# Performance work log

Hardware: AMD Instinct MI355X
Metric: run time of the kernel (lower is better)

## Reference

```python
import jax, jax.numpy as jnp
import numpy as np

B = 4        # number of point clouds (equal-size contiguous batches)
P = 8192     # points per cloud
C_IN = 64
C_OUT = 64
K = 16       # kNN neighbors (includes the point itself, as in PyG knn)
EPS = 1e-5
NEG_SLOPE = 0.2


def setup_inputs() -> dict:
    key = jax.random.key(0)
    k1, k2, k3 = jax.random.split(key, 3)
    x = jax.random.normal(k1, (B * P, C_IN), dtype=jnp.float32)
    batch = jnp.repeat(jnp.arange(B, dtype=jnp.int64), P)  # sorted, equal sizes
    W = jax.random.normal(k2, (2 * C_IN, C_OUT), dtype=jnp.float32) * (1.0 / np.sqrt(2 * C_IN))
    b = jax.random.normal(k3, (C_OUT,), dtype=jnp.float32) * 0.01
    gamma = jnp.ones((C_OUT,), dtype=jnp.float32)
    beta = jnp.zeros((C_OUT,), dtype=jnp.float32)
    return {"x": x, "batch": batch, "W": W, "b": b, "gamma": gamma, "beta": beta}


def _edgeconv(x, W, b, gamma, beta):
    xb = x.reshape(B, P, C_IN)
    # per-cloud pairwise squared distances: [B, P, P]
    sq = jnp.sum(xb * xb, axis=-1)
    d = sq[:, :, None] + sq[:, None, :] - 2.0 * jnp.einsum("bpc,bqc->bpq", xb, xb)
    # k nearest neighbors (smallest distance, self included)
    _, idx = jax.lax.top_k(-d, K)                      # [B, P, K]
    xj = jax.vmap(lambda pts, ind: pts[ind])(xb, idx)  # [B, P, K, C_IN]
    xi = xb[:, :, None, :]
    e = jnp.concatenate([jnp.broadcast_to(xi, xj.shape), xj - xi], axis=-1)  # [B,P,K,2C]
    # edge MLP: Linear -> BatchNorm1d (training-mode batch stats over all edges) -> LeakyReLU
    h = jnp.einsum("bpke,eo->bpko", e, W) + b          # [B, P, K, C_OUT]
    hf = h.reshape(-1, C_OUT)
    mean = jnp.mean(hf, axis=0)
    var = jnp.mean(hf * hf, axis=0) - mean * mean      # biased variance (torch BN)
    hn = (h - mean) * jax.lax.rsqrt(var + EPS) * gamma + beta
    a = jnp.where(hn >= 0, hn, NEG_SLOPE * hn)
    # max aggregation over neighbors
    return jnp.max(a, axis=2).reshape(B * P, C_OUT)


def reference(x, batch, W, b, gamma, beta):
    # `batch` encodes B equal-size contiguous clouds; kNN is computed per cloud.
    return _edgeconv(x, W, b, gamma, beta)
```

## Files before the change

### kernel.cpp

```cpp
#include <hip/hip_runtime.h>
#include <cfloat>

#define BATCH 4
#define P 8192
#define C 64
#define KNN 16
#define NPTS (BATCH * P)
#define NEDGE (NPTS * KNN)
#define EPSV 1e-5f
#define SLOPE 0.2f
#define NQ 2
#define QCOLS (P / NQ)
#define QCAP 8

typedef __attribute__((ext_vector_type(8))) short bf16x8;
typedef __attribute__((ext_vector_type(16))) float f32x16;


__device__ __forceinline__ unsigned short f2bf(float f) {
    unsigned u = __float_as_uint(f);
    u += 0x7FFFu + ((u >> 16) & 1u);
    return (unsigned short)(u >> 16);
}
__device__ __forceinline__ float bf2f(unsigned short s) {
    return __uint_as_float(((unsigned)s) << 16);
}
__device__ __forceinline__ unsigned monof(float f) {
    unsigned u = __float_as_uint(f);
    return u ^ ((unsigned)((int)u >> 31) | 0x80000000u);
}
__device__ __forceinline__ float invmonof(unsigned k) {
    unsigned u = (k & 0x80000000u) ? (k ^ 0x80000000u) : ~k;
    return __uint_as_float(u);
}

__global__ void prep_frag(const float* __restrict__ x, uint4* __restrict__ xfh,
                          uint4* __restrict__ xfm, uint4* __restrict__ xfl,
                          float* __restrict__ sq) {
    __shared__ float part[32][9];
    int tid = threadIdx.x;
    int ptl = tid >> 3, j8 = tid & 7;
    int g = blockIdx.x;
    int p = g * 32 + ptl;
    const float4* xp = (const float4*)(x + (size_t)p * C + j8 * 8);
    float4 a = xp[0], b = xp[1];
    float v[8] = {a.x, a.y, a.z, a.w, b.x, b.y, b.z, b.w};
    unsigned short hs[8], ms[8], ls[8];
    float ssum = 0.f;
#pragma unroll
    for (int e = 0; e < 8; ++e) {
        float xv = v[e];
        ssum = fmaf(xv, xv, ssum);
        unsigned short h = f2bf(xv);
        float r1 = xv - bf2f(h);
        unsigned short m = f2bf(r1);
        float r2 = r1 - bf2f(m);
        unsigned short l = f2bf(r2);
        hs[e] = h; ms[e] = m; ls[e] = l;
    }
    int dst = (g * 4 + (j8 >> 1)) * 64 + ptl + 32 * (j8 & 1);
    uint4 ph, pm, pl;
    ph.x = (unsigned)hs[0] | ((unsigned)hs[1] << 16);
    ph.y = (unsigned)hs[2] | ((unsigned)hs[3] << 16);
    ph.z = (unsigned)hs[4] | ((unsigned)hs[5] << 16);
    ph.w = (unsigned)hs[6] | ((unsigned)hs[7] << 16);
    pm.x = (unsigned)ms[0] | ((unsigned)ms[1] << 16);
    pm.y = (unsigned)ms[2] | ((unsigned)ms[3] << 16);
    pm.z = (unsigned)ms[4] | ((unsigned)ms[5] << 16);
    pm.w = (unsigned)ms[6] | ((unsigned)ms[7] << 16);
    pl.x = (unsigned)ls[0] | ((unsigned)ls[1] << 16);
    pl.y = (unsigned)ls[2] | ((unsigned)ls[3] << 16);
    pl.z = (unsigned)ls[4] | ((unsigned)ls[5] << 16);
    pl.w = (unsigned)ls[6] | ((unsigned)ls[7] << 16);
    xfh[dst] = ph; xfm[dst] = pm; xfl[dst] = pl;
    part[ptl][j8] = ssum;
    __syncthreads();
    if (j8 == 0) {
        float s = 0.f;
#pragma unroll
        for (int k = 0; k < 8; ++k) s += part[ptl][k];
        sq[p] = s;
    }
}

#define SORTED_INS16(MV, IDV)                                                  \
    {                                                                          \
        float _m = (MV); int _id = (IDV);                                      \
        bool c0 = _m < tv[0], c1 = _m < tv[1], c2 = _m < tv[2],                \
             c3 = _m < tv[3], c4 = _m < tv[4], c5 = _m < tv[5],                \
             c6 = _m < tv[6], c7 = _m < tv[7], c8 = _m < tv[8],                \
             c9 = _m < tv[9], c10 = _m < tv[10], c11 = _m < tv[11],            \
             c12 = _m < tv[12], c13 = _m < tv[13], c14 = _m < tv[14],          \
             c15 = _m < tv[15];                                                \
        tv[15] = c15 ? (c14 ? tv[14] : _m) : tv[15];                           \
        ti[15] = c15 ? (c14 ? ti[14] : _id) : ti[15];                          \
        tv[14] = c14 ? (c13 ? tv[13] : _m) : tv[14];                           \
        ti[14] = c14 ? (c13 ? ti[13] : _id) : ti[14];                          \
        tv[13] = c13 ? (c12 ? tv[12] : _m) : tv[13];                           \
        ti[13] = c13 ? (c12 ? ti[12] : _id) : ti[13];                          \
        tv[12] = c12 ? (c11 ? tv[11] : _m) : tv[12];                           \
        ti[12] = c12 ? (c11 ? ti[11] : _id) : ti[12];                          \
        tv[11] = c11 ? (c10 ? tv[10] : _m) : tv[11];                           \
        ti[11] = c11 ? (c10 ? ti[10] : _id) : ti[11];                          \
        tv[10] = c10 ? (c9 ? tv[9] : _m) : tv[10];                             \
        ti[10] = c10 ? (c9 ? ti[9] : _id) : ti[10];                            \
        tv[9] = c9 ? (c8 ? tv[8] : _m) : tv[9];                                \
        ti[9] = c9 ? (c8 ? ti[8] : _id) : ti[9];                               \
        tv[8] = c8 ? (c7 ? tv[7] : _m) : tv[8];                                \
        ti[8] = c8 ? (c7 ? ti[7] : _id) : ti[8];                               \
        tv[7] = c7 ? (c6 ? tv[6] : _m) : tv[7];                                \
        ti[7] = c7 ? (c6 ? ti[6] : _id) : ti[7];                               \
        tv[6] = c6 ? (c5 ? tv[5] : _m) : tv[6];                                \
        ti[6] = c6 ? (c5 ? ti[5] : _id) : ti[6];                               \
        tv[5] = c5 ? (c4 ? tv[4] : _m) : tv[5];                                \
        ti[5] = c5 ? (c4 ? ti[4] : _id) : ti[5];                               \
        tv[4] = c4 ? (c3 ? tv[3] : _m) : tv[4];                                \
        ti[4] = c4 ? (c3 ? ti[3] : _id) : ti[4];                               \
        tv[3] = c3 ? (c2 ? tv[2] : _m) : tv[3];                                \
        ti[3] = c3 ? (c2 ? ti[2] : _id) : ti[3];                               \
        tv[2] = c2 ? (c1 ? tv[1] : _m) : tv[2];                                \
        ti[2] = c2 ? (c1 ? ti[1] : _id) : ti[2];                               \
        tv[1] = c1 ? (c0 ? tv[0] : _m) : tv[1];                                \
        ti[1] = c1 ? (c0 ? ti[0] : _id) : ti[1];                               \
        tv[0] = c0 ? _m : tv[0];                                               \
        ti[0] = c0 ? _id : ti[0];                                              \
    }

#define DRAIN_Q                                                                \
    {                                                                          \
        _Pragma("nounroll")                                                    \
        for (int j = 0; j < QCAP; ++j) {                                       \
            unsigned long long kq = q[j * 256 + tid];                          \
            bool valid = (j < qn);                                             \
            float dv = valid ? __uint_as_float((unsigned)(kq >> 32)) : FLT_MAX;\
            int di = (int)(unsigned)(kq & 0xFFFFFFFFu);                        \
            SORTED_INS16(dv, di)                                               \
        }                                                                      \
        qn = 0;                                                                \
    }

__global__ __launch_bounds__(256, 4) void knn_kernel(const uint4* __restrict__ xfh,
                                                     const uint4* __restrict__ xfm,
                                                     const uint4* __restrict__ xfl,
                                                     const float* __restrict__ sq,
                                                     float* __restrict__ pv,
                                                     int* __restrict__ pi) {
    __shared__ unsigned long long smem[64 * 65];
    unsigned long long* q = smem;
    unsigned long long (*fink)[65] = (unsigned long long (*)[65])smem;

    int tid = threadIdx.x;
    int b = blockIdx.x & 3;
    int t = blockIdx.x >> 2;
    int tile = t & 127;
    int half = t >> 7;
    int bglob = b * P;
    int r0 = tile * 64;
    int w = tid >> 6, lane = tid & 63;
    int wr = w & 1, wc = w >> 1;
    int hi = lane >> 5;
    int rloc = lane & 31;

    int gA = ((bglob + r0) >> 5) + wr;
    bf16x8 Rh[4], Rm[4], Rl[4];
#pragma unroll
    for (int kk = 0; kk < 4; ++kk) {
        Rh[kk] = __builtin_bit_cast(bf16x8, xfh[(gA * 4 + kk) * 64 + lane]);
        Rm[kk] = __builtin_bit_cast(bf16x8, xfm[(gA * 4 + kk) * 64 + lane]);
        Rl[kk] = __builtin_bit_cast(bf16x8, xfl[(gA * 4 + kk) * 64 + lane]);
    }

    float tv[16];
    int   ti[16];
#pragma unroll
    for (int j = 0; j < 16; ++j) { tv[j] = FLT_MAX; ti[j] = 0; }
    int qn = 0;

    int cw0 = half * QCOLS + wc * 2048;

    for (int chunk = 0; chunk < 64; ++chunk) {
        int c0 = cw0 + chunk * 32;
        int gB = (bglob + c0) >> 5;
        const uint4* ch = &xfh[(gB * 4) * 64 + lane];
        const uint4* cm = &xfm[(gB * 4) * 64 + lane];
        const uint4* cl = &xfl[(gB * 4) * 64 + lane];

        f32x16 acc0, acc1;
#pragma unroll
        for (int i = 0; i < 16; ++i) { acc0[i] = 0.f; acc1[i] = 0.f; }
#pragma unroll
        for (int kk = 0; kk < 4; ++kk) {
            bf16x8 Ch = __builtin_bit_cast(bf16x8, ch[kk * 64]);
            bf16x8 Cm = __builtin_bit_cast(bf16x8, cm[kk * 64]);
            bf16x8 Cl = __builtin_bit_cast(bf16x8, cl[kk * 64]);
            acc0 = __builtin_amdgcn_mfma_f32_32x32x16_bf16(Ch, Rh[kk], acc0, 0, 0, 0);
            acc1 = __builtin_amdgcn_mfma_f32_32x32x16_bf16(Ch, Rm[kk], acc1, 0, 0, 0);
            acc0 = __builtin_amdgcn_mfma_f32_32x32x16_bf16(Cm, Rh[kk], acc0, 0, 0, 0);
            acc1 = __builtin_amdgcn_mfma_f32_32x32x16_bf16(Cm, Rm[kk], acc1, 0, 0, 0);
            acc0 = __builtin_amdgcn_mfma_f32_32x32x16_bf16(Ch, Rl[kk], acc0, 0, 0, 0);
            acc1 = __builtin_amdgcn_mfma_f32_32x32x16_bf16(Cl, Rh[kk], acc1, 0, 0, 0);
        }

        int cb = c0 + 4 * hi;
        float4 sqA[4];
#pragma unroll
        for (int g4 = 0; g4 < 4; ++g4)
            sqA[g4] = *(const float4*)(&sq[bglob + cb + g4 * 8]);
        int bgc = bglob + cb;

#pragma unroll
        for (int reg = 0; reg < 16; ++reg) {
            float s = fmaf(-2.f, acc0[reg] + acc1[reg],
                           ((const float*)&sqA[reg >> 2])[reg & 3]);
            if (__any(qn == QCAP)) { DRAIN_Q }
            bool pass = s < tv[15];
            if (pass) {
                int cid = bgc + (reg & 3) + 8 * (reg >> 2);
                unsigned long long kk =
                    ((unsigned long long)__float_as_uint(s) << 32) | (unsigned)cid;
                q[qn * 256 + tid] = kk;
                qn += 1;
            }
        }
    }

    DRAIN_Q

    __syncthreads();

    {
        int rowl = 32 * wr + rloc;
        int li = wc * 2 + hi;
#pragma unroll
        for (int j = 0; j < 16; ++j)
            fink[rowl][li * 16 + j] =
                ((unsigned long long)monof(tv[j]) << 32) | (unsigned)ti[j];
    }
    __syncthreads();
    if (tid < 128) {
        int row = tid & 63, pr = tid >> 6;
        int base = pr * 32;
        unsigned long long tk[16];
#pragma unroll
        for (int j = 0; j < 16; ++j) tk[j] = fink[row][base + j];
        unsigned long long worstk = tk[0];
#pragma unroll
        for (int j = 1; j < 16; ++j) worstk = (tk[j] > worstk) ? tk[j] : worstk;
        for (int e = 0; e < 16; ++e) {
            unsigned long long k = fink[row][base + 16 + e];
            if (k < worstk) {
                unsigned long long mx = tk[0]; int pos = 0;
#pragma unroll
                for (int j = 1; j < 16; ++j) {
                    bool g = tk[j] > mx; mx = g ? tk[j] : mx; pos = g ? j : pos;
                }
#pragma unroll
                for (int j = 0; j < 16; ++j)
                    if (j == pos) tk[j] = k;
                unsigned long long nw = tk[0];
#pragma unroll
                for (int j = 1; j < 16; ++j) nw = (tk[j] > nw) ? tk[j] : nw;
                worstk = nw;
            }
        }
#pragma unroll
        for (int j = 0; j < 16; ++j) fink[row][base + j] = tk[j];
    }
    __syncthreads();
    if (tid < 64) {
        int row = tid;
        unsigned long long tk[16];
#pragma unroll
        for (int j = 0; j < 16; ++j) tk[j] = fink[row][j];
        unsigned long long worstk = tk[0];
#pragma unroll
        for (int j = 1; j < 16; ++j) worstk = (tk[j] > worstk) ? tk[j] : worstk;
        for (int e = 0; e < 16; ++e) {
            unsigned long long k = fink[row][32 + e];
            if (k < worstk) {
                unsigned long long mx = tk[0]; int pos = 0;
#pragma unroll
                for (int j = 1; j < 16; ++j) {
                    bool g = tk[j] > mx; mx = g ? tk[j] : mx; pos = g ? j : pos;
                }
#pragma unroll
                for (int j = 0; j < 16; ++j)
                    if (j == pos) tk[j] = k;
                unsigned long long nw = tk[0];
#pragma unroll
                for (int j = 1; j < 16; ++j) nw = (tk[j] > nw) ? tk[j] : nw;
                worstk = nw;
            }
        }
        size_t o = (((size_t)(bglob + r0 + row)) * NQ + half) * KNN;
#pragma unroll
        for (int j = 0; j < 16; ++j) {
            pv[o + j] = invmonof((unsigned)(tk[j] >> 32));
            pi[o + j] = (int)(unsigned)(tk[j] & 0xFFFFFFFFu);
        }
    }
}

__global__ void merge_kernel(const float* __restrict__ pv, const int* __restrict__ pi,
                             int* __restrict__ idx_out) {
    __shared__ unsigned long long mk[128 * 33];
    int tid = threadIdx.x;
    int lr = tid & 127, q = tid >> 7;
    int row = blockIdx.x * 128 + lr;
    size_t o = ((size_t)row * NQ + q) * KNN;
#pragma unroll
    for (int j = 0; j < 16; ++j) {
        mk[lr * 33 + q * 16 + j] =
            ((unsigned long long)monof(pv[o + j]) << 32) | (unsigned)pi[o + j];
    }
    __syncthreads();
    if (tid < 128) {
        unsigned long long tk[16];
#pragma unroll
        for (int j = 0; j < 16; ++j) tk[j] = mk[tid * 33 + j];
        unsigned long long worstk = tk[0];
#pragma unroll
        for (int j = 1; j < 16; ++j) worstk = (tk[j] > worstk) ? tk[j] : worstk;
        for (int e = 16; e < 32; ++e) {
            unsigned long long k = mk[tid * 33 + e];
            if (k < worstk) {
                unsigned long long mx = tk[0]; int pos = 0;
#pragma unroll
                for (int j = 1; j < 16; ++j) {
                    bool g = tk[j] > mx; mx = g ? tk[j] : mx; pos = g ? j : pos;
                }
#pragma unroll
                for (int j = 0; j < 16; ++j)
                    if (j == pos) tk[j] = k;
                unsigned long long nw = tk[0];
#pragma unroll
                for (int j = 1; j < 16; ++j) nw = (tk[j] > nw) ? tk[j] : nw;
                worstk = nw;
            }
        }
        size_t oo = (size_t)tid * KNN + (size_t)blockIdx.x * 128 * KNN;
#pragma unroll
        for (int j = 0; j < 16; ++j)
            idx_out[oo + j] = (int)(unsigned)(tk[j] & 0xFFFFFFFFu);
    }
}

__global__ void prep_UV(const float* __restrict__ x, const float* __restrict__ W,
                        float* __restrict__ U, float* __restrict__ V) {
    __shared__ float Ws[128][64];
    __shared__ float xs[4][64];
    int tid = threadIdx.x;
    for (int i = tid; i < 128 * 64; i += 256) ((float*)Ws)[i] = W[i];
    int p0 = blockIdx.x * 4;
    int r = tid >> 6, c = tid & 63;
    xs[r][c] = x[(size_t)(p0 + r) * C + c];
    __syncthreads();
    float u = 0.f, v = 0.f;
#pragma unroll
    for (int k = 0; k < 64; ++k) {
        float xv = xs[r][k];
        float w1 = Ws[k][c];
        float w2 = Ws[64 + k][c];
        u = fmaf(xv, w1 - w2, u);
        v = fmaf(xv, w2, v);
    }
    size_t o = (size_t)(p0 + r) * C + c;
    U[o] = u;
    V[o] = v;
}

__global__ void stats_kernel(const float* __restrict__ U, const float* __restrict__ V,
                             const float* __restrict__ bias, const int* __restrict__ idx,
                             float* __restrict__ stats) {
    int tid = threadIdx.x;
    int c = tid & 63, kk = tid >> 6;
    int p0 = blockIdx.x * 32;
    float bc = bias[c];
    float sum = 0.f, sumsq = 0.f;
    for (int pp = 0; pp < 32; ++pp) {
        int p = p0 + pp;
        float u = U[(size_t)p * C + c] + bc;
#pragma unroll
        for (int k4 = 0; k4 < 4; ++k4) {
            int j = idx[(size_t)p * KNN + kk * 4 + k4];
            float h = u + V[(size_t)j * C + c];
            sum += h;
            sumsq = fmaf(h, h, sumsq);
        }
    }
    __shared__ float red[2][4][64];
    red[0][kk][c] = sum;
    red[1][kk][c] = sumsq;
    __syncthreads();
    if (tid < 64) {
        float s = red[0][0][tid] + red[0][1][tid] + red[0][2][tid] + red[0][3][tid];
        atomicAdd(&stats[tid], s);
    } else if (tid < 128) {
        int cc = tid - 64;
        float s = red[1][0][cc] + red[1][1][cc] + red[1][2][cc] + red[1][3][cc];
        atomicAdd(&stats[64 + cc], s);
    }
}

__global__ void finalize_kernel(const float* __restrict__ stats,
                                const float* __restrict__ gamma,
                                const float* __restrict__ beta,
                                float* __restrict__ sshift) {
    int c = threadIdx.x;
    const float N = (float)NEDGE;
    float mean = stats[c] / N;
    float var = stats[64 + c] / N - mean * mean;
    float s = gamma[c] * rsqrtf(var + EPSV);
    sshift[c] = s;
    sshift[64 + c] = beta[c] - mean * s;
}

__global__ void out_kernel(const float* __restrict__ U, const float* __restrict__ V,
                           const float* __restrict__ bias, const int* __restrict__ idx,
                           const float* __restrict__ sshift, float* __restrict__ out) {
    int tid = threadIdx.x;
    int c = tid & 63, g = tid >> 6;
    int p0 = blockIdx.x * 16;
    float s = sshift[c], t = sshift[64 + c];
    float bc = bias[c];
    for (int pp = g; pp < 16; pp += 4) {
        int p = p0 + pp;
        float mx = -FLT_MAX, mn = FLT_MAX;
#pragma unroll
        for (int k = 0; k < KNN; ++k) {
            int j = idx[(size_t)p * KNN + k];
            float v = V[(size_t)j * C + c];
            mx = fmaxf(mx, v);
            mn = fminf(mn, v);
        }
        float hsel = (s >= 0.f) ? mx : mn;
        float hn = fmaf(s, U[(size_t)p * C + c] + bc + hsel, t);
        out[(size_t)p * C + c] = (hn >= 0.f) ? hn : SLOPE * hn;
    }
}

extern "C" void kernel_launch(void* const* d_in, const int* in_sizes, int n_in,
                              void* d_out, int out_size, void* d_ws, size_t ws_size,
                              hipStream_t stream) {
    const float* x     = (const float*)d_in[0];
    const float* W     = (const float*)d_in[2];
    const float* bias  = (const float*)d_in[3];
    const float* gamma = (const float*)d_in[4];
    const float* beta  = (const float*)d_in[5];
    float* out = (float*)d_out;

    float* wsf    = (float*)d_ws;
    float* U      = wsf;
    float* V      = wsf + 2097152;
    uint4* xfh    = (uint4*)wsf;
    uint4* xfm    = (uint4*)(wsf + 1048576);
    uint4* xfl    = (uint4*)(wsf + 2097152);
    float* sq     = wsf + 4194304;
    float* stats  = wsf + 4227072;
    float* sshift = wsf + 4227200;
    int*   idx    = (int*)(wsf + 4227328);
    float* pv     = wsf + 4751616;
    int*   pi     = (int*)(wsf + 5800192);

    hipLaunchKernelGGL(prep_frag, dim3(NPTS / 32), dim3(256), 0, stream, x, xfh, xfm, xfl, sq);
    hipLaunchKernelGGL(knn_kernel, dim3(BATCH * (P / 64) * NQ), dim3(256), 0, stream,
                       (const uint4*)xfh, (const uint4*)xfm, (const uint4*)xfl, sq, pv, pi);
    hipLaunchKernelGGL(merge_kernel, dim3(NPTS / 128), dim3(256), 0, stream, pv, pi, idx);
    hipLaunchKernelGGL(prep_UV, dim3(NPTS / 4), dim3(256), 0, stream, x, W, U, V);
    hipMemsetAsync(stats, 0, 128 * sizeof(float), stream);
    hipLaunchKernelGGL(stats_kernel, dim3(NPTS / 32), dim3(256), 0, stream, U, V, bias, idx, stats);
    hipLaunchKernelGGL(finalize_kernel, dim3(1), dim3(64), 0, stream, stats, gamma, beta, sshift);
    hipLaunchKernelGGL(out_kernel, dim3(NPTS / 16), dim3(256), 0, stream, U, V, bias, idx, sshift, out);
}
```

Baseline: 509.7 us.

## Compute neighbor max/min during stats pass and fold finalize into output kernel

The stats kernel now also tracks per-channel max and min of the gathered V values over the 16 neighbors and writes the pre-normalization selected value to a buffer. It picks max or min from the sign of gamma, since the rsqrt factor is positive. The output kernel no longer re-gathers V through idx. It becomes an elementwise float4 normalize plus LeakyReLU, and each block recomputes the scale and shift itself, which removes the separate finalize launch. In exchange it writes and reads an extra 8 MB hsel buffer, which reuses the pv workspace region.

```diff
diff --git a/kernel.cpp b/kernel.cpp
--- a/kernel.cpp
+++ b/kernel.cpp
@@ -370,27 +370,35 @@
 }
 
 __global__ void stats_kernel(const float* __restrict__ U, const float* __restrict__ V,
-                             const float* __restrict__ bias, const int* __restrict__ idx,
-                             float* __restrict__ stats) {
-    int tid = threadIdx.x;
-    int c = tid & 63, kk = tid >> 6;
+                             const float* __restrict__ bias,
+                             const float* __restrict__ gamma,
+                             const int* __restrict__ idx,
+                             float* __restrict__ stats, float* __restrict__ hsel) {
+    int tid = threadIdx.x;
+    int c = tid & 63, g = tid >> 6;
     int p0 = blockIdx.x * 32;
     float bc = bias[c];
+    bool gpos = (gamma[c] >= 0.f);
     float sum = 0.f, sumsq = 0.f;
-    for (int pp = 0; pp < 32; ++pp) {
+    for (int pp = g; pp < 32; pp += 4) {
         int p = p0 + pp;
         float u = U[(size_t)p * C + c] + bc;
-#pragma unroll
-        for (int k4 = 0; k4 < 4; ++k4) {
-            int j = idx[(size_t)p * KNN + kk * 4 + k4];
-            float h = u + V[(size_t)j * C + c];
+        float mx = -FLT_MAX, mn = FLT_MAX;
+#pragma unroll
+        for (int k = 0; k < KNN; ++k) {
+            int j = idx[(size_t)p * KNN + k];
+            float v = V[(size_t)j * C + c];
+            float h = u + v;
             sum += h;
             sumsq = fmaf(h, h, sumsq);
-        }
+            mx = fmaxf(mx, v);
+            mn = fminf(mn, v);
+        }
+        hsel[(size_t)p * C + c] = u + (gpos ? mx : mn);
     }
     __shared__ float red[2][4][64];
-    red[0][kk][c] = sum;
-    red[1][kk][c] = sumsq;
+    red[0][g][c] = sum;
+    red[1][g][c] = sumsq;
     __syncthreads();
     if (tid < 64) {
         float s = red[0][0][tid] + red[0][1][tid] + red[0][2][tid] + red[0][3][tid];
@@ -402,40 +410,38 @@
     }
 }
 
-__global__ void finalize_kernel(const float* __restrict__ stats,
-                                const float* __restrict__ gamma,
-                                const float* __restrict__ beta,
-                                float* __restrict__ sshift) {
-    int c = threadIdx.x;
-    const float N = (float)NEDGE;
-    float mean = stats[c] / N;
-    float var = stats[64 + c] / N - mean * mean;
-    float s = gamma[c] * rsqrtf(var + EPSV);
-    sshift[c] = s;
-    sshift[64 + c] = beta[c] - mean * s;
-}
-
-__global__ void out_kernel(const float* __restrict__ U, const float* __restrict__ V,
-                           const float* __restrict__ bias, const int* __restrict__ idx,
-                           const float* __restrict__ sshift, float* __restrict__ out) {
-    int tid = threadIdx.x;
-    int c = tid & 63, g = tid >> 6;
-    int p0 = blockIdx.x * 16;
-    float s = sshift[c], t = sshift[64 + c];
-    float bc = bias[c];
-    for (int pp = g; pp < 16; pp += 4) {
-        int p = p0 + pp;
-        float mx = -FLT_MAX, mn = FLT_MAX;
-#pragma unroll
-        for (int k = 0; k < KNN; ++k) {
-            int j = idx[(size_t)p * KNN + k];
-            float v = V[(size_t)j * C + c];
-            mx = fmaxf(mx, v);
-            mn = fminf(mn, v);
-        }
-        float hsel = (s >= 0.f) ? mx : mn;
-        float hn = fmaf(s, U[(size_t)p * C + c] + bc + hsel, t);
-        out[(size_t)p * C + c] = (hn >= 0.f) ? hn : SLOPE * hn;
+__global__ void out_kernel(const float* __restrict__ hsel,
+                           const float* __restrict__ stats,
+                           const float* __restrict__ gamma,
+                           const float* __restrict__ beta,
+                           float* __restrict__ out) {
+    __shared__ float sS[64], sT[64];
+    int tid = threadIdx.x;
+    if (tid < 64) {
+        const float N = (float)NEDGE;
+        float mean = stats[tid] / N;
+        float var = stats[64 + tid] / N - mean * mean;
+        float s = gamma[tid] * rsqrtf(var + EPSV);
+        sS[tid] = s;
+        sT[tid] = beta[tid] - mean * s;
+    }
+    __syncthreads();
+    int gid = blockIdx.x * 256 + tid;
+#pragma unroll
+    for (int r = 0; r < 2; ++r) {
+        size_t i4 = (size_t)gid + (size_t)r * 262144;
+        size_t i = i4 * 4;
+        int c0 = (int)(i & 63);
+        float4 h4 = *(const float4*)&hsel[i];
+        float4 s4 = *(const float4*)&sS[c0];
+        float4 t4 = *(const float4*)&sT[c0];
+        float4 o4;
+        float hn;
+        hn = fmaf(s4.x, h4.x, t4.x); o4.x = (hn >= 0.f) ? hn : SLOPE * hn;
+        hn = fmaf(s4.y, h4.y, t4.y); o4.y = (hn >= 0.f) ? hn : SLOPE * hn;
+        hn = fmaf(s4.z, h4.z, t4.z); o4.z = (hn >= 0.f) ? hn : SLOPE * hn;
+        hn = fmaf(s4.w, h4.w, t4.w); o4.w = (hn >= 0.f) ? hn : SLOPE * hn;
+        *(float4*)&out[i] = o4;
     }
 }
 
@@ -457,10 +463,10 @@
     uint4* xfl    = (uint4*)(wsf + 2097152);
     float* sq     = wsf + 4194304;
     float* stats  = wsf + 4227072;
-    float* sshift = wsf + 4227200;
     int*   idx    = (int*)(wsf + 4227328);
     float* pv     = wsf + 4751616;
     int*   pi     = (int*)(wsf + 5800192);
+    float* hsel   = wsf + 4751616;
 
     hipLaunchKernelGGL(prep_frag, dim3(NPTS / 32), dim3(256), 0, stream, x, xfh, xfm, xfl, sq);
     hipLaunchKernelGGL(knn_kernel, dim3(BATCH * (P / 64) * NQ), dim3(256), 0, stream,
@@ -468,7 +474,8 @@
     hipLaunchKernelGGL(merge_kernel, dim3(NPTS / 128), dim3(256), 0, stream, pv, pi, idx);
     hipLaunchKernelGGL(prep_UV, dim3(NPTS / 4), dim3(256), 0, stream, x, W, U, V);
     hipMemsetAsync(stats, 0, 128 * sizeof(float), stream);
-    hipLaunchKernelGGL(stats_kernel, dim3(NPTS / 32), dim3(256), 0, stream, U, V, bias, idx, stats);
-    hipLaunchKernelGGL(finalize_kernel, dim3(1), dim3(64), 0, stream, stats, gamma, beta, sshift);
-    hipLaunchKernelGGL(out_kernel, dim3(NPTS / 16), dim3(256), 0, stream, U, V, bias, idx, sshift, out);
-}
+    hipLaunchKernelGGL(stats_kernel, dim3(NPTS / 32), dim3(256), 0, stream,
+                       U, V, bias, gamma, idx, stats, hsel);
+    hipLaunchKernelGGL(out_kernel, dim3(1024), dim3(256), 0, stream,
+                       hsel, stats, gamma, beta, out);
+}
```

After: 501.5 us. No clear change (-1.6%).
